# Optimization experiments

Hardware: AMD Instinct MI355X
Metric: run time of the kernel (lower is better)

## Reference

```python
import jax, jax.numpy as jnp
from jax import lax
import numpy as np

P = 9          # patch_size (hardcoded in CUTSEncoder)
HALF = P // 2  # 4
EPS = 1e-5     # BatchNorm eps (torch default)
SLOPE = 0.01   # LeakyReLU negative slope (torch default)


def _conv(x, w, b):
    # 3x3 'same' conv, NCHW / OIHW
    y = lax.conv_general_dilated(x, w, (1, 1), 'SAME',
                                 dimension_numbers=('NCHW', 'OIHW', 'NCHW'))
    return y + b[None, :, None, None]


def _bn(x, gamma, beta):
    # training-mode BatchNorm2d: batch statistics over (N,H,W)
    m = jnp.mean(x, axis=(0, 2, 3), keepdims=True)
    v = jnp.var(x, axis=(0, 2, 3), keepdims=True)
    return gamma[None, :, None, None] * (x - m) * lax.rsqrt(v + EPS) + beta[None, :, None, None]


def _block(x, w, b, g, be):
    return jax.nn.leaky_relu(_bn(_conv(x, w, b), g, be), SLOPE)


def setup_inputs() -> dict:
    key = jax.random.key(0)
    ks = jax.random.split(key, 16)
    B, C, H, W = 8, 3, 256, 256
    K = 32                 # num_kernels
    L = K * 8              # latent_dim = 256
    S = 32                 # sampled_patches_per_image

    x = jax.random.normal(ks[0], (B, C, H, W), jnp.float32)
    anchors_hw = jax.random.randint(ks[1], (B, S, 2), HALF, H - HALF, jnp.int32)
    positives_hw = jax.random.randint(ks[2], (B, S, 2), HALF, H - HALF, jnp.int32)

    def w_(k, shape):
        return jax.random.normal(k, shape, jnp.float32) * 0.05

    params = {
        'w1': w_(ks[3], (K, C, 3, 3)),       'b1': jnp.zeros((K,), jnp.float32),
        'g1': jnp.ones((K,), jnp.float32),   'be1': jnp.zeros((K,), jnp.float32),
        'w2': w_(ks[4], (2 * K, K, 3, 3)),   'b2': jnp.zeros((2 * K,), jnp.float32),
        'g2': jnp.ones((2 * K,), jnp.float32), 'be2': jnp.zeros((2 * K,), jnp.float32),
        'w3': w_(ks[5], (4 * K, 2 * K, 3, 3)), 'b3': jnp.zeros((4 * K,), jnp.float32),
        'g3': jnp.ones((4 * K,), jnp.float32), 'be3': jnp.zeros((4 * K,), jnp.float32),
        'w4': w_(ks[6], (8 * K, 4 * K, 3, 3)), 'b4': jnp.zeros((8 * K,), jnp.float32),
        'g4': jnp.ones((8 * K,), jnp.float32), 'be4': jnp.zeros((8 * K,), jnp.float32),
        'rw': w_(ks[7], (S * C * P * P, S * L)),  # recon Linear [out,in]
        'rb': jnp.zeros((S * C * P * P,), jnp.float32),
    }
    return dict(x=x, anchors_hw=anchors_hw, positives_hw=positives_hw, **params)


def reference(x, anchors_hw, positives_hw,
              w1, b1, g1, be1, w2, b2, g2, be2,
              w3, b3, g3, be3, w4, b4, g4, be4, rw, rb):
    B, C, H, W = x.shape
    # 4-stage conv+BN+LeakyReLU backbone -> z: [B, L, H, W]
    z = _block(x, w1, b1, g1, be1)
    z = _block(z, w2, b2, g2, be2)
    z = _block(z, w3, b3, g3, be3)
    z = _block(z, w4, b4, g4, be4)

    # batched 9x9 patch extraction around anchors: [B, S, C, P, P]
    def patch(img, hw):  # img: [C,H,W], hw: [2]
        return lax.dynamic_slice(img, (0, hw[0] - HALF, hw[1] - HALF), (C, P, P))
    x_anchors = jax.vmap(lambda img, hws: jax.vmap(lambda hw: patch(img, hw))(hws))(x, anchors_hw)

    # batched pointwise latent gathers: [B, S, L]
    def gather_z(zb, hws):  # zb: [L,H,W]
        return zb[:, hws[:, 0], hws[:, 1]].T  # [S, L]
    z_anchors = jax.vmap(gather_z)(z, anchors_hw)
    z_positives = jax.vmap(gather_z)(z, positives_hw)

    x_anchors_flat = x_anchors.reshape(B, -1)
    x_recon = z_anchors.reshape(B, -1) @ rw.T + rb
    return (z, x_anchors_flat, x_recon, z_anchors, z_positives)
```

## Files before the change

kernel.cpp:

```cpp
#include <hip/hip_runtime.h>
#include <hip/hip_bf16.h>

#define HW 65536
constexpr int IMG_W = 256;

typedef __attribute__((ext_vector_type(8))) short short8;
typedef __attribute__((ext_vector_type(4))) float f32x4;

__device__ __forceinline__ float bf2f(unsigned short u) {
    return __uint_as_float(((unsigned)u) << 16);
}
__device__ __forceinline__ unsigned short f2bf(float f) {
    __hip_bfloat16 h = __float2bfloat16(f);
    return *reinterpret_cast<unsigned short*>(&h);
}

__global__ __launch_bounds__(256) void conv1_direct(
    const float* __restrict__ x, const float* __restrict__ wt,
    const float* __restrict__ bias, unsigned short* __restrict__ outraw)
{
    constexpr int CIN = 3, COUT = 32, OCB = 16;
    const int tile = blockIdx.x;
    const int ty0 = (tile >> 3) << 5;
    const int tx0 = (tile & 7) << 5;
    const int oc0 = blockIdx.y * OCB;
    const int b = blockIdx.z;

    __shared__ alignas(16) float s_in[CIN][34][36];
    __shared__ alignas(16) float s_w[CIN][9][OCB];

    const int tid = threadIdx.x;
    const int lx = tid & 31;
    const int ly = tid >> 5;

    float acc[4][OCB];
    #pragma unroll
    for (int j = 0; j < 4; ++j)
        #pragma unroll
        for (int oc = 0; oc < OCB; ++oc) acc[j][oc] = 0.f;

    for (int idx = tid; idx < CIN * 34 * 34; idx += 256) {
        int ic  = idx / (34 * 34);
        int rem = idx - ic * (34 * 34);
        int r   = rem / 34;
        int cc  = rem - r * 34;
        int gy = ty0 - 1 + r, gx = tx0 - 1 + cc;
        float v = 0.f;
        if ((unsigned)gy < 256u && (unsigned)gx < 256u)
            v = x[((size_t)(b * CIN + ic)) * HW + (size_t)gy * IMG_W + gx];
        s_in[ic][r][cc] = v;
    }
    for (int idx = tid; idx < CIN * 9 * OCB; idx += 256) {
        int oc  = idx & (OCB - 1);
        int t2  = idx >> 4;
        int tap = t2 % 9;
        int ic  = t2 / 9;
        s_w[ic][tap][oc] = wt[((size_t)(oc0 + oc) * CIN + ic) * 9 + tap];
    }
    __syncthreads();

    for (int ic = 0; ic < CIN; ++ic) {
        #pragma unroll
        for (int tap = 0; tap < 9; ++tap) {
            const int dy = tap / 3, dx = tap % 3;
            float wr[OCB];
            #pragma unroll
            for (int q = 0; q < OCB / 4; ++q)
                *(float4*)&wr[q * 4] = *(const float4*)&s_w[ic][tap][q * 4];
            #pragma unroll
            for (int j = 0; j < 4; ++j) {
                float iv = s_in[ic][ly + 8 * j + dy][lx + dx];
                #pragma unroll
                for (int oc = 0; oc < OCB; ++oc) acc[j][oc] += iv * wr[oc];
            }
        }
    }

    #pragma unroll
    for (int j = 0; j < 4; ++j) {
        const size_t p = ((size_t)b << 16) + (size_t)((ty0 + ly + 8 * j) << 8) + tx0 + lx;
        short8 v0, v1;
        #pragma unroll
        for (int k = 0; k < 8; ++k) {
            v0[k] = (short)f2bf(acc[j][k] + bias[oc0 + k]);
            v1[k] = (short)f2bf(acc[j][8 + k] + bias[oc0 + 8 + k]);
        }
        *(short8*)&outraw[p * COUT + oc0]     = v0;
        *(short8*)&outraw[p * COUT + oc0 + 8] = v1;
    }
}

__global__ void repack2(const float* __restrict__ w, unsigned short* __restrict__ wp,
                        int COUT, int CIN)
{
    int i = blockIdx.x * 256 + threadIdx.x;
    int K9 = 9 * CIN;
    if (i >= COUT * K9) return;
    int oc = i / K9, k = i - oc * K9;
    int tap = k / CIN, ic = k - tap * CIN;
    wp[(size_t)(k >> 3) * COUT * 8 + oc * 8 + (k & 7)] =
        f2bf(w[((size_t)(oc * CIN + ic)) * 9 + tap]);
}

template<int CIN, int COUT, int NOC>
__global__ __launch_bounds__(256, 3) void conv_mfma8(
    const unsigned short* __restrict__ in, const float2* __restrict__ coef,
    const unsigned short* __restrict__ wp, const float* __restrict__ bias,
    unsigned short* __restrict__ outraw, float2* __restrict__ partial)
{
    constexpr int NG = 4;
    constexpr int CH = (CIN < 64) ? CIN : 64;
    constexpr int KH = CIN / CH;
    constexpr int CINP = CH + 8;
    constexpr int NOCT = CH / 8;
    constexpr int ICB = CH / 32;
    constexpr int TILES = 256;
    constexpr int NCH = 18 * 18 * NOCT;

    __shared__ alignas(16) short s_in[18 * 18 * CINP];
    __shared__ float2 s_coef[CIN];

    const int bx = blockIdx.x;
    const int tile = bx / NOC;
    const int oc0 = (bx - tile * NOC) * 64;
    const int b = blockIdx.z;
    const int ty0 = (tile >> 4) << 4;
    const int tx0 = (tile & 15) << 4;
    const int tid = threadIdx.x;

    if (tid < CIN) s_coef[tid] = coef[tid];

    const int lane = tid & 63;
    const int wm = tid >> 6;
    const int ln = lane & 15;
    const int grp = lane >> 4;

    f32x4 acc[4][NG] = {};

    const size_t bbase = (size_t)b << 16;
    const unsigned short* wpb = wp + ((size_t)grp * COUT + oc0 + ln) * 8;
    const int fb = (wm * 4) * 18 + ln;

    for (int kh = 0; kh < KH; ++kh) {
        __syncthreads();

        for (int idx = tid; idx < NCH; idx += 256) {
            const int ic8 = idx & (NOCT - 1);
            const int rc  = idx / NOCT;
            const int c = rc % 18, r = rc / 18;
            const int gy = ty0 - 1 + r, gx = tx0 - 1 + c;
            short8 v = (short8)0;
            if ((unsigned)gy < 256u && (unsigned)gx < 256u) {
                short8 rawv = *(const short8*)&in[(bbase + (size_t)(gy << 8) + gx) * CIN
                                                  + kh * CH + ic8 * 8];
                #pragma unroll
                for (int j = 0; j < 8; ++j) {
                    float2 ab = s_coef[kh * CH + ic8 * 8 + j];
                    float xv = fmaf(ab.x, bf2f((unsigned short)rawv[j]), ab.y);
                    xv = fmaxf(xv, 0.01f * xv);
                    v[j] = (short)f2bf(xv);
                }
            }
            *(short8*)&s_in[(r * 18 + c) * CINP + ic8 * 8] = v;
        }
        __syncthreads();

        #pragma unroll
        for (int icb = 0; icb < ICB; ++icb) {
            const int ko = icb * 32 + grp * 8;
            #pragma unroll
            for (int dx = 0; dx < 3; ++dx) {
                short8 frag[6];
                #pragma unroll
                for (int r = 0; r < 6; ++r)
                    frag[r] = *(const short8*)&s_in[(fb + r * 18 + dx) * CINP + ko];
                #pragma unroll
                for (int dy = 0; dy < 3; ++dy) {
                    const int kc0 = (dy * 3 + dx) * (CIN / 8) + kh * (CH / 8) + icb * 4;
                    short8 wfr[NG];
                    #pragma unroll
                    for (int g = 0; g < NG; ++g)
                        wfr[g] = *(const short8*)&wpb[((size_t)kc0 * COUT + g * 16) * 8];
                    #pragma unroll
                    for (int f = 0; f < 4; ++f) {
                        #pragma unroll
                        for (int g = 0; g < NG; ++g)
                            acc[f][g] = __builtin_amdgcn_mfma_f32_16x16x32_bf16(
                                wfr[g], frag[dy + f], acc[f][g], 0, 0, 0);
                    }
                }
            }
        }
    }

    const size_t pchunk = ((size_t)(b * TILES + tile) * 4 + wm) * COUT;
    #pragma unroll
    for (int g = 0; g < NG; ++g) {
        const int ocl = oc0 + g * 16 + grp * 4;
        const f32x4 b4 = *(const f32x4*)&bias[ocl];
        f32x4 vs = {}, vq = {};
        #pragma unroll
        for (int f = 0; f < 4; ++f) {
            const int row = ty0 + wm * 4 + f;
            f32x4 v = acc[f][g] + b4;
            vs += v; vq += v * v;
            short4 sv;
            sv.x = (short)f2bf(v[0]); sv.y = (short)f2bf(v[1]);
            sv.z = (short)f2bf(v[2]); sv.w = (short)f2bf(v[3]);
            *(short4*)&outraw[(bbase + (size_t)(row << 8) + tx0 + ln) * COUT + ocl] = sv;
        }
        #pragma unroll
        for (int d = 1; d < 16; d <<= 1) {
            #pragma unroll
            for (int r = 0; r < 4; ++r) {
                vs[r] += __shfl_xor(vs[r], d);
                vq[r] += __shfl_xor(vq[r], d);
            }
        }
        if (ln == 0) {
            #pragma unroll
            for (int r = 0; r < 4; ++r)
                partial[pchunk + ocl + r] = make_float2(vs[r], vq[r]);
        }
    }
}

template<int C>
__global__ __launch_bounds__(256) void bn_stats_nhwc(const unsigned short* __restrict__ raw,
                                                     float2* __restrict__ partial)
{
    constexpr int CPT = C / 8;
    constexpr int PPI = 256 / CPT;
    const int t = threadIdx.x;
    const int co = t % CPT, pg = t / CPT;
    const int p0 = blockIdx.x * 2048;
    float s[8], ss[8];
    #pragma unroll
    for (int j = 0; j < 8; ++j) { s[j] = 0.f; ss[j] = 0.f; }
    for (int p = p0 + pg; p < p0 + 2048; p += PPI) {
        short8 v = *(const short8*)&raw[(size_t)p * C + co * 8];
        #pragma unroll
        for (int j = 0; j < 8; ++j) {
            float xv = bf2f((unsigned short)v[j]);
            s[j] += xv; ss[j] += xv * xv;
        }
    }
    __shared__ float rs[256][8], rss[256][8];
    #pragma unroll
    for (int j = 0; j < 8; ++j) { rs[t][j] = s[j]; rss[t][j] = ss[j]; }
    __syncthreads();
    for (int off = PPI / 2; off > 0; off >>= 1) {
        if (pg < off) {
            #pragma unroll
            for (int j = 0; j < 8; ++j) {
                rs[t][j]  += rs[t + off * CPT][j];
                rss[t][j] += rss[t + off * CPT][j];
            }
        }
        __syncthreads();
    }
    if (pg == 0) {
        #pragma unroll
        for (int j = 0; j < 8; ++j)
            partial[(size_t)(co * 8 + j) * 256 + blockIdx.x] = make_float2(rs[t][j], rss[t][j]);
    }
}

__global__ void bn_finalize_kernel(const float2* __restrict__ partial,
                                   const float* __restrict__ gamma,
                                   const float* __restrict__ beta,
                                   float2* __restrict__ coef, int C, int nchunk)
{
    int c = threadIdx.x;
    if (c >= C) return;
    float s = 0.f, ss = 0.f;
    for (int i = 0; i < nchunk; ++i) {
        float2 p = partial[(size_t)c * nchunk + i];
        s += p.x; ss += p.y;
    }
    const float N = 524288.f;
    float m = s / N;
    float v = ss / N - m * m;
    float rsq = rsqrtf(v + 1e-5f);
    float a = gamma[c] * rsq;
    coef[c] = make_float2(a, beta[c] - m * a);
}

template<int C, int NCHUNK>
__global__ __launch_bounds__(256) void bn_finalize3(const float2* __restrict__ partial,
                                                    const float* __restrict__ gamma,
                                                    const float* __restrict__ beta,
                                                    float2* __restrict__ coef)
{
    const int c = blockIdx.x, t = threadIdx.x;
    float s = 0.f, q = 0.f;
    for (int i = t; i < NCHUNK; i += 256) {
        float2 p = partial[(size_t)i * C + c];
        s += p.x; q += p.y;
    }
    __shared__ float rs[256], rq[256];
    rs[t] = s; rq[t] = q;
    __syncthreads();
    for (int off = 128; off; off >>= 1) {
        if (t < off) { rs[t] += rs[t + off]; rq[t] += rq[t + off]; }
        __syncthreads();
    }
    if (t == 0) {
        const float N = 524288.f;
        float m = rs[0] / N;
        float v = rq[0] / N - m * m;
        float a = gamma[c] * rsqrtf(v + 1e-5f);
        coef[c] = make_float2(a, beta[c] - m * a);
    }
}

__global__ __launch_bounds__(256) void apply_t(const unsigned short* __restrict__ raw,
                                               const float2* __restrict__ coef,
                                               float* __restrict__ z)
{
    __shared__ float s_t[256 * 36];
    __shared__ float2 s_c[256];
    const int t = threadIdx.x;
    s_c[t] = coef[t];
    __syncthreads();

    const size_t p0 = (size_t)blockIdx.x * 32;
    const int o = t & 31, prow = t >> 5;
    #pragma unroll
    for (int it = 0; it < 4; ++it) {
        const int pxi = prow + it * 8;
        short8 v = *(const short8*)&raw[(p0 + pxi) * 256 + o * 8];
        #pragma unroll
        for (int j = 0; j < 8; ++j) {
            const int oc = o * 8 + j;
            float2 ab = s_c[oc];
            float xv = fmaf(ab.x, bf2f((unsigned short)v[j]), ab.y);
            xv = fmaxf(xv, 0.01f * xv);
            s_t[oc * 36 + (pxi ^ ((o & 7) * 4))] = xv;
        }
    }
    __syncthreads();

    const int Q = t & 7, ocr = t >> 3;
    const int b = (int)(p0 >> 16);
    const int pxl = (int)(p0 & 65535);
    #pragma unroll
    for (int pass = 0; pass < 8; ++pass) {
        const int oc = ocr + pass * 32;
        const int w = (oc >> 3) & 7;
        f32x4 vv = *(const f32x4*)&s_t[oc * 36 + ((Q ^ w) * 4)];
        *(f32x4*)&z[(((size_t)(b * 256 + oc)) << 16) + pxl + Q * 4] = vv;
    }
}

__global__ void patches_kernel(const float* __restrict__ x, const int* __restrict__ hw,
                               float* __restrict__ out)
{
    int bs = blockIdx.x;
    int b = bs >> 5;
    int h = hw[bs * 2], w = hw[bs * 2 + 1];
    int t = threadIdx.x;
    if (t < 243) {
        int c = t / 81, r = (t / 9) % 9, cc = t % 9;
        out[(size_t)bs * 243 + t] =
            x[((size_t)(b * 3 + c)) * HW + (size_t)(h - 4 + r) * IMG_W + (w - 4 + cc)];
    }
}

__global__ void gather_kernel(const float* __restrict__ z, const int* __restrict__ hw,
                              float* __restrict__ out)
{
    int bs = blockIdx.x;
    int b = bs >> 5;
    int h = hw[bs * 2], w = hw[bs * 2 + 1];
    int l = threadIdx.x;
    out[(size_t)bs * 256 + l] = z[((size_t)(b * 256 + l)) * HW + (size_t)h * IMG_W + w];
}

__global__ __launch_bounds__(256) void recon_kernel(const float* __restrict__ za,
                                                    const float* __restrict__ rw,
                                                    const float* __restrict__ rb,
                                                    float* __restrict__ out)
{
    int wave = threadIdx.x >> 6, lane = threadIdx.x & 63;
    int n0 = blockIdx.x * 16 + wave * 4;
    float acc[4][8];
    #pragma unroll
    for (int j = 0; j < 4; ++j)
        #pragma unroll
        for (int bb = 0; bb < 8; ++bb) acc[j][bb] = 0.f;

    for (int i = 0; i < 32; ++i) {
        int k = i * 256 + lane * 4;
        float4 wv[4];
        #pragma unroll
        for (int j = 0; j < 4; ++j)
            wv[j] = *(const float4*)&rw[(size_t)(n0 + j) * 8192 + k];
        #pragma unroll
        for (int bb = 0; bb < 8; ++bb) {
            float4 zv = *(const float4*)&za[(size_t)bb * 8192 + k];
            #pragma unroll
            for (int j = 0; j < 4; ++j)
                acc[j][bb] += zv.x * wv[j].x + zv.y * wv[j].y + zv.z * wv[j].z + zv.w * wv[j].w;
        }
    }
    #pragma unroll
    for (int j = 0; j < 4; ++j)
        #pragma unroll
        for (int bb = 0; bb < 8; ++bb) {
            float v = acc[j][bb];
            #pragma unroll
            for (int off = 32; off; off >>= 1) v += __shfl_down(v, off);
            if (lane == 0) out[(size_t)bb * 7776 + n0 + j] = v + rb[n0 + j];
        }
}

extern "C" void kernel_launch(void* const* d_in, const int* in_sizes, int n_in,
                              void* d_out, int out_size, void* d_ws, size_t ws_size,
                              hipStream_t stream) {
    (void)in_sizes; (void)n_in; (void)out_size; (void)ws_size;

    const float* x        = (const float*)d_in[0];
    const int* anchors    = (const int*)d_in[1];
    const int* positives  = (const int*)d_in[2];
    const float* w1 = (const float*)d_in[3];  const float* b1 = (const float*)d_in[4];
    const float* g1 = (const float*)d_in[5];  const float* be1 = (const float*)d_in[6];
    const float* w2 = (const float*)d_in[7];  const float* b2 = (const float*)d_in[8];
    const float* g2 = (const float*)d_in[9];  const float* be2 = (const float*)d_in[10];
    const float* w3 = (const float*)d_in[11]; const float* b3 = (const float*)d_in[12];
    const float* g3 = (const float*)d_in[13]; const float* be3 = (const float*)d_in[14];
    const float* w4 = (const float*)d_in[15]; const float* b4 = (const float*)d_in[16];
    const float* g4 = (const float*)d_in[17]; const float* be4 = (const float*)d_in[18];
    const float* rw = (const float*)d_in[19]; const float* rb = (const float*)d_in[20];

    float* z  = (float*)d_out;
    float* xa = z + 134217728;
    float* xr = xa + 62208;
    float* za = xr + 62208;
    float* zp = za + 65536;

    char* zb = (char*)d_out;
    unsigned short* raw1 = (unsigned short*)zb;
    unsigned short* raw2 = (unsigned short*)(zb + 33554432ull);
    unsigned short* raw3 = (unsigned short*)(zb + 100663296ull);

    char* ws = (char*)d_ws;
    unsigned short* wp   = (unsigned short*)ws;
    float2* partial = (float2*)(ws + 1048576ull);
    float2* coef1   = (float2*)(ws + 17825792ull);
    float2* coef2   = coef1 + 256;
    float2* coef3   = coef2 + 256;
    float2* coef4   = coef3 + 256;
    unsigned short* raw4 = (unsigned short*)(ws + 18874368ull);

    conv1_direct<<<dim3(64, 2, 8), 256, 0, stream>>>(x, w1, b1, raw1);
    bn_stats_nhwc<32><<<256, 256, 0, stream>>>(raw1, partial);
    bn_finalize_kernel<<<1, 256, 0, stream>>>(partial, g1, be1, coef1, 32, 256);

    repack2<<<(64 * 288 + 255) / 256, 256, 0, stream>>>(w2, wp, 64, 32);
    conv_mfma8<32, 64, 1><<<dim3(256, 1, 8), 256, 0, stream>>>(raw1, coef1, wp, b2, raw2, partial);
    bn_finalize3<64, 8192><<<64, 256, 0, stream>>>(partial, g2, be2, coef2);

    repack2<<<(128 * 576 + 255) / 256, 256, 0, stream>>>(w3, wp, 128, 64);
    conv_mfma8<64, 128, 2><<<dim3(512, 1, 8), 256, 0, stream>>>(raw2, coef2, wp, b3, raw3, partial);
    bn_finalize3<128, 8192><<<128, 256, 0, stream>>>(partial, g3, be3, coef3);

    repack2<<<(256 * 1152 + 255) / 256, 256, 0, stream>>>(w4, wp, 256, 128);
    conv_mfma8<128, 256, 4><<<dim3(1024, 1, 8), 256, 0, stream>>>(raw3, coef3, wp, b4, raw4, partial);
    bn_finalize3<256, 8192><<<256, 256, 0, stream>>>(partial, g4, be4, coef4);

    apply_t<<<16384, 256, 0, stream>>>(raw4, coef4, z);

    patches_kernel<<<256, 256, 0, stream>>>(x, anchors, xa);
    gather_kernel<<<256, 256, 0, stream>>>(z, anchors, za);
    gather_kernel<<<256, 256, 0, stream>>>(z, positives, zp);
    recon_kernel<<<486, 256, 0, stream>>>(za, rw, rb, xr);
}
```

Measured before the change: 934.7 us.

## Stage conv weights in LDS and retile MFMA conv to 8x16 pixels with 2D warp split

```diff
diff --git a/kernel.cpp b/kernel.cpp
--- a/kernel.cpp
+++ b/kernel.cpp
@@ -90,63 +90,75 @@
     }
 }
 
-__global__ void repack2(const float* __restrict__ w, unsigned short* __restrict__ wp,
-                        int COUT, int CIN)
-{
+__global__ void repack3(const float* __restrict__ w, unsigned short* __restrict__ wp,
+                        int COUT, int CIN, int OCB)
+{
+    const int CH = CIN < 64 ? CIN : 64;
+    const int KH = CIN / CH;
+    const int ICQ = CH / 8;
+    const int total = COUT * CIN * 9;
     int i = blockIdx.x * 256 + threadIdx.x;
-    int K9 = 9 * CIN;
-    if (i >= COUT * K9) return;
-    int oc = i / K9, k = i - oc * K9;
-    int tap = k / CIN, ic = k - tap * CIN;
-    wp[(size_t)(k >> 3) * COUT * 8 + oc * 8 + (k & 7)] =
-        f2bf(w[((size_t)(oc * CIN + ic)) * 9 + tap]);
-}
-
-template<int CIN, int COUT, int NOC>
-__global__ __launch_bounds__(256, 3) void conv_mfma8(
+    if (i >= total) return;
+    int s = i;
+    int j   = s & 7;    s >>= 3;
+    int ocl = s % OCB;  s /= OCB;
+    int icq = s % ICQ;  s /= ICQ;
+    int dy  = s % 3;    s /= 3;
+    int kh  = s % KH;   s /= KH;
+    int dx  = s % 3;
+    int ocb = s / 3;
+    int oc = ocb * OCB + ocl;
+    int ic = kh * CH + icq * 8 + j;
+    wp[i] = f2bf(w[((size_t)(oc * CIN + ic)) * 9 + dy * 3 + dx]);
+}
+
+template<int CIN, int COUT, int OCB, int NOC, int MINW>
+__global__ __launch_bounds__(256, MINW) void conv_mfma9(
     const unsigned short* __restrict__ in, const float2* __restrict__ coef,
     const unsigned short* __restrict__ wp, const float* __restrict__ bias,
     unsigned short* __restrict__ outraw, float2* __restrict__ partial)
 {
-    constexpr int NG = 4;
+    constexpr int WOC = OCB / 2;
+    constexpr int NG = WOC / 16;
     constexpr int CH = (CIN < 64) ? CIN : 64;
     constexpr int KH = CIN / CH;
     constexpr int CINP = CH + 8;
-    constexpr int NOCT = CH / 8;
     constexpr int ICB = CH / 32;
-    constexpr int TILES = 256;
-    constexpr int NCH = 18 * 18 * NOCT;
-
-    __shared__ alignas(16) short s_in[18 * 18 * CINP];
+    constexpr int ICQ = CH / 8;
+    constexpr int SLAB = 3 * ICQ * OCB * 8;
+    constexpr int WCH = SLAB / 8;
+    constexpr int NCHI = 10 * 18 * ICQ;
+
+    __shared__ alignas(16) short s_in[10 * 18 * CINP];
+    __shared__ alignas(16) short s_w[SLAB];
     __shared__ float2 s_coef[CIN];
 
     const int bx = blockIdx.x;
-    const int tile = bx / NOC;
-    const int oc0 = (bx - tile * NOC) * 64;
+    int tile, ocb;
+    if (NOC == 2) { tile = ((bx >> 4) << 3) | (bx & 7); ocb = (bx >> 3) & 1; }
+    else          { tile = bx; ocb = 0; }
     const int b = blockIdx.z;
-    const int ty0 = (tile >> 4) << 4;
+    const int ty0 = (tile >> 4) << 3;
     const int tx0 = (tile & 15) << 4;
     const int tid = threadIdx.x;
 
     if (tid < CIN) s_coef[tid] = coef[tid];
+    __syncthreads();
 
     const int lane = tid & 63;
-    const int wm = tid >> 6;
+    const int wv = tid >> 6;
+    const int wm = wv >> 1, wn = wv & 1;
     const int ln = lane & 15;
     const int grp = lane >> 4;
 
     f32x4 acc[4][NG] = {};
-
     const size_t bbase = (size_t)b << 16;
-    const unsigned short* wpb = wp + ((size_t)grp * COUT + oc0 + ln) * 8;
     const int fb = (wm * 4) * 18 + ln;
 
     for (int kh = 0; kh < KH; ++kh) {
-        __syncthreads();
-
-        for (int idx = tid; idx < NCH; idx += 256) {
-            const int ic8 = idx & (NOCT - 1);
-            const int rc  = idx / NOCT;
+        for (int idx = tid; idx < NCHI; idx += 256) {
+            const int ic8 = idx & (ICQ - 1);
+            const int rc  = idx / ICQ;
             const int c = rc % 18, r = rc / 18;
             const int gy = ty0 - 1 + r, gx = tx0 - 1 + c;
             short8 v = (short8)0;
@@ -163,41 +175,43 @@
             }
             *(short8*)&s_in[(r * 18 + c) * CINP + ic8 * 8] = v;
         }
-        __syncthreads();
-
-        #pragma unroll
-        for (int icb = 0; icb < ICB; ++icb) {
-            const int ko = icb * 32 + grp * 8;
-            #pragma unroll
-            for (int dx = 0; dx < 3; ++dx) {
+
+        for (int dx = 0; dx < 3; ++dx) {
+            const unsigned short* wsrc = wp + (size_t)((ocb * 3 + dx) * KH + kh) * SLAB;
+            for (int i = tid; i < WCH; i += 256)
+                *(short8*)&s_w[i * 8] = *(const short8*)&wsrc[(size_t)i * 8];
+            __syncthreads();
+
+            #pragma unroll
+            for (int icb = 0; icb < ICB; ++icb) {
                 short8 frag[6];
                 #pragma unroll
                 for (int r = 0; r < 6; ++r)
-                    frag[r] = *(const short8*)&s_in[(fb + r * 18 + dx) * CINP + ko];
+                    frag[r] = *(const short8*)&s_in[(fb + r * 18 + dx) * CINP + icb * 32 + grp * 8];
                 #pragma unroll
                 for (int dy = 0; dy < 3; ++dy) {
-                    const int kc0 = (dy * 3 + dx) * (CIN / 8) + kh * (CH / 8) + icb * 4;
                     short8 wfr[NG];
                     #pragma unroll
                     for (int g = 0; g < NG; ++g)
-                        wfr[g] = *(const short8*)&wpb[((size_t)kc0 * COUT + g * 16) * 8];
+                        wfr[g] = *(const short8*)&s_w[((dy * ICQ + icb * 4 + grp) * OCB
+                                                      + wn * WOC + g * 16 + ln) * 8];
                     #pragma unroll
-                    for (int f = 0; f < 4; ++f) {
+                    for (int f = 0; f < 4; ++f)
                         #pragma unroll
                         for (int g = 0; g < NG; ++g)
                             acc[f][g] = __builtin_amdgcn_mfma_f32_16x16x32_bf16(
                                 wfr[g], frag[dy + f], acc[f][g], 0, 0, 0);
-                    }
                 }
             }
-        }
-    }
-
-    const size_t pchunk = ((size_t)(b * TILES + tile) * 4 + wm) * COUT;
+            __syncthreads();
+        }
+    }
+
+    const size_t pchunk = ((size_t)(b * 512 + tile) * 2 + wm) * COUT;
     #pragma unroll
     for (int g = 0; g < NG; ++g) {
-        const int ocl = oc0 + g * 16 + grp * 4;
-        const f32x4 b4 = *(const f32x4*)&bias[ocl];
+        const int ocg = ocb * OCB + wn * WOC + g * 16 + grp * 4;
+        const f32x4 b4 = *(const f32x4*)&bias[ocg];
         f32x4 vs = {}, vq = {};
         #pragma unroll
         for (int f = 0; f < 4; ++f) {
@@ -207,7 +221,7 @@
             short4 sv;
             sv.x = (short)f2bf(v[0]); sv.y = (short)f2bf(v[1]);
             sv.z = (short)f2bf(v[2]); sv.w = (short)f2bf(v[3]);
-            *(short4*)&outraw[(bbase + (size_t)(row << 8) + tx0 + ln) * COUT + ocl] = sv;
+            *(short4*)&outraw[(bbase + (size_t)(row << 8) + tx0 + ln) * COUT + ocg] = sv;
         }
         #pragma unroll
         for (int d = 1; d < 16; d <<= 1) {
@@ -220,7 +234,7 @@
         if (ln == 0) {
             #pragma unroll
             for (int r = 0; r < 4; ++r)
-                partial[pchunk + ocl + r] = make_float2(vs[r], vq[r]);
+                partial[pchunk + ocg + r] = make_float2(vs[r], vq[r]);
         }
     }
 }
@@ -457,16 +471,16 @@
     bn_stats_nhwc<32><<<256, 256, 0, stream>>>(raw1, partial);
     bn_finalize_kernel<<<1, 256, 0, stream>>>(partial, g1, be1, coef1, 32, 256);
 
-    repack2<<<(64 * 288 + 255) / 256, 256, 0, stream>>>(w2, wp, 64, 32);
-    conv_mfma8<32, 64, 1><<<dim3(256, 1, 8), 256, 0, stream>>>(raw1, coef1, wp, b2, raw2, partial);
+    repack3<<<(64 * 288 + 255) / 256, 256, 0, stream>>>(w2, wp, 64, 32, 64);
+    conv_mfma9<32, 64, 64, 1, 3><<<dim3(512, 1, 8), 256, 0, stream>>>(raw1, coef1, wp, b2, raw2, partial);
     bn_finalize3<64, 8192><<<64, 256, 0, stream>>>(partial, g2, be2, coef2);
 
-    repack2<<<(128 * 576 + 255) / 256, 256, 0, stream>>>(w3, wp, 128, 64);
-    conv_mfma8<64, 128, 2><<<dim3(512, 1, 8), 256, 0, stream>>>(raw2, coef2, wp, b3, raw3, partial);
+    repack3<<<(128 * 576 + 255) / 256, 256, 0, stream>>>(w3, wp, 128, 64, 128);
+    conv_mfma9<64, 128, 128, 1, 2><<<dim3(512, 1, 8), 256, 0, stream>>>(raw2, coef2, wp, b3, raw3, partial);
     bn_finalize3<128, 8192><<<128, 256, 0, stream>>>(partial, g3, be3, coef3);
 
-    repack2<<<(256 * 1152 + 255) / 256, 256, 0, stream>>>(w4, wp, 256, 128);
-    conv_mfma8<128, 256, 4><<<dim3(1024, 1, 8), 256, 0, stream>>>(raw3, coef3, wp, b4, raw4, partial);
+    repack3<<<(256 * 1152 + 255) / 256, 256, 0, stream>>>(w4, wp, 256, 128, 128);
+    conv_mfma9<128, 256, 128, 2, 2><<<dim3(1024, 1, 8), 256, 0, stream>>>(raw3, coef3, wp, b4, raw4, partial);
     bn_finalize3<256, 8192><<<256, 256, 0, stream>>>(partial, g4, be4, coef4);
 
     apply_t<<<16384, 256, 0, stream>>>(raw4, coef4, z);
```

After: 1.058 ms. +13.2%, slower.
